# Optimization experiments

Hardware: AMD Instinct MI355X
Metric: run time of the kernel (lower is better)

Reference implementation:

```python
import jax, jax.numpy as jnp
import numpy as np
import math

N_HEAD = 16

def _rope_tables(seq, dh, dtype):
    inv_freq = 1.0 / (10000.0 ** (jnp.arange(0, dh, 2, dtype=jnp.float32) / dh))
    angle = jnp.arange(seq, dtype=jnp.float32)[:, None] * inv_freq[None, :]  # [S, dh/2]
    sin = jnp.repeat(jnp.sin(angle), 2, axis=-1).astype(dtype)  # [S, dh]
    cos = jnp.repeat(jnp.cos(angle), 2, axis=-1).astype(dtype)
    return sin, cos

def _rotate_half(x):
    x_even = x[..., ::2]
    x_odd = x[..., 1::2]
    return jnp.stack([-x_odd, x_even], axis=-1).reshape(x.shape)

def _apply_rope(x, sin, cos):
    # x: [B, H, S, dh]; sin/cos: [S, dh]
    return x * cos[None, None] + _rotate_half(x) * sin[None, None]

def setup_inputs() -> dict:
    key = jax.random.key(0)
    ks = jax.random.split(key, 9)
    B, S, D = 2, 2048, 2048
    scale = 1.0 / math.sqrt(D)
    x = jax.random.normal(ks[0], (B, S, D), dtype=jnp.float32)
    wq = jax.random.normal(ks[1], (D, D), dtype=jnp.float32) * scale
    wk = jax.random.normal(ks[2], (D, D), dtype=jnp.float32) * scale
    wv = jax.random.normal(ks[3], (D, D), dtype=jnp.float32) * scale
    wo = jax.random.normal(ks[4], (D, D), dtype=jnp.float32) * scale
    bq = jnp.zeros((D,), jnp.float32)
    bk = jnp.zeros((D,), jnp.float32)
    bv = jnp.zeros((D,), jnp.float32)
    bo = jnp.zeros((D,), jnp.float32)
    # causal mask: True = masked (strict upper triangle)
    mask = jnp.triu(jnp.ones((S, S), dtype=bool), k=1)[None, None]  # [1,1,S,S]
    return {"x": x, "wq": wq, "bq": bq, "wk": wk, "bk": bk, "wv": wv, "bv": bv,
            "wo": wo, "bo": bo, "mask": mask}

def reference(x, wq, bq, wk, bk, wv, bv, wo, bo, mask):
    B, S, D = x.shape
    H = N_HEAD
    dh = D // H
    # projections (torch Linear: x @ W.T + b)
    q = (x @ wq.T + bq).reshape(B, S, H, dh).transpose(0, 2, 1, 3)  # [B,H,S,dh]
    k = (x @ wk.T + bk).reshape(B, S, H, dh).transpose(0, 2, 1, 3)
    v = (x @ wv.T + bv).reshape(B, S, H, dh).transpose(0, 2, 1, 3)
    sin, cos = _rope_tables(S, dh, x.dtype)
    q = _apply_rope(q, sin, cos)
    k = _apply_rope(k, sin, cos)
    scores = jnp.einsum('bhqd,bhkd->bhqk', q, k) / math.sqrt(dh)
    scores = jnp.where(mask, -jnp.inf, scores)
    attn = jax.nn.softmax(scores, axis=-1)
    attn = jnp.nan_to_num(attn, nan=0.0)
    out = jnp.einsum('bhqk,bhkd->bhqd', attn, v)  # [B,H,S,dh]
    out = out.transpose(0, 2, 1, 3).reshape(B, S, D)
    return out @ wo.T + bo
```

## Files before the change

kernel.cpp:

```cpp
#include <hip/hip_runtime.h>
#include <math.h>


typedef _Float16 half8 __attribute__((ext_vector_type(8)));
typedef _Float16 half4v __attribute__((ext_vector_type(4)));
typedef float f32x4 __attribute__((ext_vector_type(4)));

__device__ __forceinline__ void gl_lds16(const void* g, void* l) {
  __builtin_amdgcn_global_load_lds(
      (const __attribute__((address_space(1))) unsigned int*)g,
      (__attribute__((address_space(3))) unsigned int*)l, 16, 0, 0);
}

__global__ void cast_f32_f16(const float* __restrict__ src, _Float16* __restrict__ dst, int n4) {
  int i = blockIdx.x * blockDim.x + threadIdx.x;
  if (i >= n4) return;
  float4 v = reinterpret_cast<const float4*>(src)[i];
  half4v o;
  o[0] = (_Float16)v.x; o[1] = (_Float16)v.y; o[2] = (_Float16)v.z; o[3] = (_Float16)v.w;
  reinterpret_cast<half4v*>(dst)[i] = o;
}

__global__ void cast_w(const float* __restrict__ w0, const float* __restrict__ w1,
                       const float* __restrict__ w2, const float* __restrict__ w3,
                       _Float16* __restrict__ wdst) {
  const float* s = blockIdx.y == 0 ? w0 : blockIdx.y == 1 ? w1 : blockIdx.y == 2 ? w2 : w3;
  int i = blockIdx.x * blockDim.x + threadIdx.x;
  float4 v = reinterpret_cast<const float4*>(s)[i];
  half4v o;
  o[0] = (_Float16)v.x; o[1] = (_Float16)v.y; o[2] = (_Float16)v.z; o[3] = (_Float16)v.w;
  reinterpret_cast<half4v*>(wdst)[(size_t)blockIdx.y * 1048576 + i] = o;
}

template <bool OUT_F32>
__global__ __launch_bounds__(256, 2) void gemm_bt(
    const _Float16* __restrict__ A,
    const _Float16* __restrict__ B,
    const float* __restrict__ b0, const float* __restrict__ b1,
    const float* __restrict__ b2,
    void* __restrict__ Cout,
    int M, int N, int K) {
  __shared__ _Float16 As[2][4096];
  __shared__ _Float16 Bs[2][4096];
  const int bm = blockIdx.y * 128, bn = blockIdx.x * 128;
  const int tid = threadIdx.x;
  const int wave = tid >> 6, lane = tid & 63;
  const int quad = lane >> 4, l16 = lane & 15;
  const int hh = wave >> 1, gg = wave & 1;

  const _Float16* gsrc[4];
  int lofs[4];
#pragma unroll
  for (int p = 0; p < 4; ++p) {
    int c = ((p & 1) * 256 + tid) & 511;
    int cl16 = c & 15, cqd = (c >> 4) & 3, ci = (c >> 6) & 3, ch = c >> 8;
    int grow = ch * 64 + ci * 16 + cl16;
    int gcol = cqd * 8;
    gsrc[p] = (p < 2 ? A + (size_t)(bm + grow) * K : B + (size_t)(bn + grow) * K) + gcol;
    lofs[p] = c * 8;
  }

  f32x4 acc[4][4];
#pragma unroll
  for (int i = 0; i < 4; ++i)
#pragma unroll
    for (int n = 0; n < 4; ++n) acc[i][n] = f32x4{0.f, 0.f, 0.f, 0.f};

#pragma unroll
  for (int p = 0; p < 4; ++p)
    gl_lds16(gsrc[p], (p < 2 ? &As[0][lofs[p]] : &Bs[0][lofs[p]]));

  const int nit = K >> 5;
  for (int it = 0; it < nit; ++it) {
    __syncthreads();
    const int cur = it & 1;
    if (it + 1 < nit) {
      const int nxt = cur ^ 1, ko = (it + 1) * 32;
#pragma unroll
      for (int p = 0; p < 4; ++p)
        gl_lds16(gsrc[p] + ko, (p < 2 ? &As[nxt][lofs[p]] : &Bs[nxt][lofs[p]]));
    }
    half8 af[4], bf[4];
#pragma unroll
    for (int i = 0; i < 4; ++i)
      af[i] = *reinterpret_cast<const half8*>(&As[cur][((hh * 4 + i) * 4 + quad) * 128 + l16 * 8]);
#pragma unroll
    for (int n = 0; n < 4; ++n)
      bf[n] = *reinterpret_cast<const half8*>(&Bs[cur][((gg * 4 + n) * 4 + quad) * 128 + l16 * 8]);
#pragma unroll
    for (int i = 0; i < 4; ++i)
#pragma unroll
      for (int n = 0; n < 4; ++n)
        acc[i][n] = __builtin_amdgcn_mfma_f32_16x16x32_f16(af[i], bf[n], acc[i][n], 0, 0, 0);
  }

  const int wm = hh * 64, wn = gg * 64;
#pragma unroll
  for (int n = 0; n < 4; ++n) {
    const int gc = bn + wn + n * 16 + l16;
    const float* bp = (gc < 2048) ? b0 : (gc < 4096 ? b1 : b2);
    const float bz = bp[gc & 2047];
#pragma unroll
    for (int i = 0; i < 4; ++i) {
#pragma unroll
      for (int r = 0; r < 4; ++r) {
        const int gr = bm + wm + i * 16 + quad * 4 + r;
        float v = acc[i][n][r] + bz;
        if (OUT_F32)
          reinterpret_cast<float*>(Cout)[(size_t)gr * N + gc] = v;
        else
          reinterpret_cast<_Float16*>(Cout)[(size_t)gr * N + gc] = (_Float16)v;
      }
    }
  }
}

__global__ void rope_inplace(_Float16* __restrict__ qkv, int ngroups) {
  int idx = blockIdx.x * blockDim.x + threadIdx.x;
  if (idx >= ngroups) return;
  int m = idx >> 8;
  int g = idx & 255;
  int s = m & 2047;
  const float scale = 0.088388347648318447f;
  size_t base = (size_t)m * 6144 + g * 8;
  half8 qv = *reinterpret_cast<const half8*>(qkv + base);
  half8 kv = *reinterpret_cast<const half8*>(qkv + base + 2048);
  half8 qo, ko;
#pragma unroll
  for (int j = 0; j < 4; ++j) {
    int i = (g * 4 + j) & 63;
    float ang = (float)s * exp2f(-0.2076205059304601f * (float)i);
    float sn, cs;
    __sincosf(ang, &sn, &cs);
    float e = (float)qv[j * 2], o = (float)qv[j * 2 + 1];
    qo[j * 2]     = (_Float16)((e * cs - o * sn) * scale);
    qo[j * 2 + 1] = (_Float16)((o * cs + e * sn) * scale);
    e = (float)kv[j * 2]; o = (float)kv[j * 2 + 1];
    ko[j * 2]     = (_Float16)(e * cs - o * sn);
    ko[j * 2 + 1] = (_Float16)(o * cs + e * sn);
  }
  *reinterpret_cast<half8*>(qkv + base) = qo;
  *reinterpret_cast<half8*>(qkv + base + 2048) = ko;
}

__global__ __launch_bounds__(256) void transpose_v(const _Float16* __restrict__ qkv,
                                                   _Float16* __restrict__ vt) {
  __shared__ _Float16 t[64][72];
  const int s0 = blockIdx.x * 64;
  const int d0 = blockIdx.y * 64;
  const int bh = blockIdx.z;
  const int b = bh >> 4, h = bh & 15;
  const int tid = threadIdx.x;
#pragma unroll
  for (int p = 0; p < 2; ++p) {
    int chunk = p * 256 + tid;
    int r = chunk >> 3, c8 = (chunk & 7) * 8;
    *reinterpret_cast<half8*>(&t[r][c8]) = *reinterpret_cast<const half8*>(
        &qkv[(size_t)(b * 2048 + s0 + r) * 6144 + 4096 + h * 128 + d0 + c8]);
  }
  __syncthreads();
#pragma unroll
  for (int p = 0; p < 2; ++p) {
    int chunk = p * 256 + tid;
    int dr = chunk >> 3, c8 = (chunk & 7) * 8;
    half8 o;
#pragma unroll
    for (int j = 0; j < 8; ++j) o[j] = t[c8 + j][dr];
    *reinterpret_cast<half8*>(&vt[(size_t)(bh * 128 + d0 + dr) * 2048 + s0 + c8]) = o;
  }
}

__global__ __launch_bounds__(256, 2) void attn_kernel(
    const _Float16* __restrict__ QKV,
    const _Float16* __restrict__ VT,
    _Float16* __restrict__ ctx) {
  constexpr int LD = 6144, S = 2048;
  __shared__ _Float16 Ks[2][8192];
  __shared__ _Float16 Vs[2][8192];
  __shared__ _Float16 P[4][16][80];
  const int bid = blockIdx.x;
  const int bh = bid & 31;
  const int qt = 31 - (bid >> 5);
  const int b = bh >> 4, h = bh & 15;
  const int tid = threadIdx.x;
  const int wv = tid >> 6, lane = tid & 63;
  const int quad = lane >> 4, l16 = lane & 15;
  const int q0 = qt * 64 + wv * 16;

  const _Float16* qp = QKV + (size_t)(b * S + q0 + l16) * LD + h * 128;
  half8 aq[4];
#pragma unroll
  for (int ks = 0; ks < 4; ++ks)
    aq[ks] = *reinterpret_cast<const half8*>(qp + ks * 32 + quad * 8);

  const _Float16* gk[4];
  const _Float16* gv[4];
  int lofs[4];
#pragma unroll
  for (int p = 0; p < 4; ++p) {
    int c = p * 256 + tid;
    int cl16 = c & 15, cqd = (c >> 4) & 3;
    int cks = (c >> 6) & 3, cf = c >> 8;
    gk[p] = QKV + (size_t)(b * S + cf * 16 + cl16) * LD + 2048 + h * 128 + cks * 32 + cqd * 8;
    int ckv = (c >> 6) & 1, ct = c >> 7;
    gv[p] = VT + (size_t)(bh * 128 + ct * 16 + cl16) * S + ckv * 32 + cqd * 8;
    lofs[p] = c * 8;
  }

  f32x4 acc[8];
#pragma unroll
  for (int t = 0; t < 8; ++t) acc[t] = f32x4{0.f, 0.f, 0.f, 0.f};
  f32x4 lacc = f32x4{0.f, 0.f, 0.f, 0.f};
  float m_i[4];
#pragma unroll
  for (int r = 0; r < 4; ++r) m_i[r] = -INFINITY;

  half8 ones;
#pragma unroll
  for (int j = 0; j < 8; ++j) ones[j] = (_Float16)1.0f;

#pragma unroll
  for (int p = 0; p < 4; ++p) gl_lds16(gk[p], &Ks[0][lofs[p]]);
#pragma unroll
  for (int p = 0; p < 4; ++p) gl_lds16(gv[p], &Vs[0][lofs[p]]);

  for (int j = 0; j <= qt; ++j) {
    __syncthreads();
    const int cur = j & 1;
    if (j < qt) {
      const size_t ko = (size_t)(j + 1) * 64 * LD;
      const int vo = (j + 1) * 64;
#pragma unroll
      for (int p = 0; p < 4; ++p) gl_lds16(gk[p] + ko, &Ks[cur ^ 1][lofs[p]]);
#pragma unroll
      for (int p = 0; p < 4; ++p) gl_lds16(gv[p] + vo, &Vs[cur ^ 1][lofs[p]]);
    }
    f32x4 sf[4];
#pragma unroll
    for (int f = 0; f < 4; ++f) sf[f] = f32x4{0.f, 0.f, 0.f, 0.f};
#pragma unroll
    for (int f = 0; f < 4; ++f)
#pragma unroll
      for (int ks = 0; ks < 4; ++ks) {
        half8 bk = *reinterpret_cast<const half8*>(&Ks[cur][((f * 4 + ks) * 4 + quad) * 128 + l16 * 8]);
        sf[f] = __builtin_amdgcn_mfma_f32_16x16x32_f16(aq[ks], bk, sf[f], 0, 0, 0);
      }
    if (j == qt) {
      const int key0 = j * 64;
#pragma unroll
      for (int f = 0; f < 4; ++f) {
        const int key = key0 + f * 16 + l16;
#pragma unroll
        for (int r = 0; r < 4; ++r) {
          const int row = q0 + quad * 4 + r;
          sf[f][r] = (key <= row) ? sf[f][r] : -1e30f;
        }
      }
    }
    float alpha[4];
#pragma unroll
    for (int r = 0; r < 4; ++r) {
      float tm = fmaxf(fmaxf(sf[0][r], sf[1][r]), fmaxf(sf[2][r], sf[3][r]));
      tm = fmaxf(tm, __shfl_xor(tm, 1));
      tm = fmaxf(tm, __shfl_xor(tm, 2));
      tm = fmaxf(tm, __shfl_xor(tm, 4));
      tm = fmaxf(tm, __shfl_xor(tm, 8));
      const float mn = fmaxf(m_i[r], tm);
      alpha[r] = __expf(m_i[r] - mn);
      m_i[r] = mn;
    }
#pragma unroll
    for (int f = 0; f < 4; ++f)
#pragma unroll
      for (int r = 0; r < 4; ++r)
        P[wv][quad * 4 + r][f * 16 + l16] = (_Float16)__expf(sf[f][r] - m_i[r]);
    half8 pa0 = *reinterpret_cast<const half8*>(&P[wv][l16][quad * 8]);
    half8 pa1 = *reinterpret_cast<const half8*>(&P[wv][l16][32 + quad * 8]);
#pragma unroll
    for (int t = 0; t < 8; ++t)
#pragma unroll
      for (int r = 0; r < 4; ++r) acc[t][r] *= alpha[r];
#pragma unroll
    for (int r = 0; r < 4; ++r) lacc[r] *= alpha[r];
#pragma unroll
    for (int t = 0; t < 8; ++t) {
      half8 bv0 = *reinterpret_cast<const half8*>(&Vs[cur][((t * 2 + 0) * 4 + quad) * 128 + l16 * 8]);
      half8 bv1 = *reinterpret_cast<const half8*>(&Vs[cur][((t * 2 + 1) * 4 + quad) * 128 + l16 * 8]);
      acc[t] = __builtin_amdgcn_mfma_f32_16x16x32_f16(pa0, bv0, acc[t], 0, 0, 0);
      acc[t] = __builtin_amdgcn_mfma_f32_16x16x32_f16(pa1, bv1, acc[t], 0, 0, 0);
    }
    lacc = __builtin_amdgcn_mfma_f32_16x16x32_f16(pa0, ones, lacc, 0, 0, 0);
    lacc = __builtin_amdgcn_mfma_f32_16x16x32_f16(pa1, ones, lacc, 0, 0, 0);
  }

  float inv[4];
#pragma unroll
  for (int r = 0; r < 4; ++r) inv[r] = 1.0f / lacc[r];
#pragma unroll
  for (int t = 0; t < 8; ++t)
#pragma unroll
    for (int r = 0; r < 4; ++r)
      ctx[(size_t)(b * S + q0 + quad * 4 + r) * 2048 + h * 128 + t * 16 + l16] =
          (_Float16)(acc[t][r] * inv[r]);
}

extern "C" void kernel_launch(void* const* d_in, const int* in_sizes, int n_in,
                              void* d_out, int out_size, void* d_ws, size_t ws_size,
                              hipStream_t stream) {
  const float* x  = (const float*)d_in[0];
  const float* wq = (const float*)d_in[1];
  const float* bq = (const float*)d_in[2];
  const float* wk = (const float*)d_in[3];
  const float* bk = (const float*)d_in[4];
  const float* wv = (const float*)d_in[5];
  const float* bv = (const float*)d_in[6];
  const float* wo = (const float*)d_in[7];
  const float* bo = (const float*)d_in[8];

  _Float16* W      = (_Float16*)d_ws;
  _Float16* xh     = W;
  _Float16* wqkvh  = xh + 8388608;
  _Float16* woh    = wqkvh + 12582912;
  _Float16* qkvlin = woh + 4194304;
  _Float16* vT     = xh;
  _Float16* ctx    = wqkvh;

  cast_f32_f16<<<8192, 256, 0, stream>>>(x, xh, 2097152);
  cast_w<<<dim3(4096, 4), 256, 0, stream>>>(wq, wk, wv, wo, wqkvh);

  gemm_bt<false><<<dim3(48, 32), 256, 0, stream>>>(xh, wqkvh, bq, bk, bv, qkvlin,
                                                   4096, 6144, 2048);

  rope_inplace<<<4096, 256, 0, stream>>>(qkvlin, 1048576);
  transpose_v<<<dim3(32, 2, 32), 256, 0, stream>>>(qkvlin, vT);
  attn_kernel<<<1024, 256, 0, stream>>>(qkvlin, vT, ctx);

  gemm_bt<true><<<dim3(16, 32), 256, 0, stream>>>(ctx, woh, bo, bo, bo, (float*)d_out,
                                                  4096, 2048, 2048);
}
```

Before: 518.9 us.

## Widen QKV GEMM tile to 128x256 and double attention query rows per block

Adds a gemm_bt_big kernel for the QKV projection that uses a 128x256 output tile, with each wave computing a 64x128 sub-tile (4x8 MFMA fragments). This raises operand reuse from LDS and halves the number of blocks. The attention kernel now gives each wave two 16-row query tiles, so each block covers 128 queries over 512 blocks and every K/V tile loaded into LDS feeds twice as many MFMAs. The trade-off is higher register pressure, fewer blocks (worse causal load balance and tail effects), and waves that skip fully masked key tiles while still taking part in the shared loads.

```diff
diff --git a/kernel.cpp b/kernel.cpp
--- a/kernel.cpp
+++ b/kernel.cpp
@@ -33,7 +33,7 @@
 }
 
 template <bool OUT_F32>
-__global__ __launch_bounds__(256, 2) void gemm_bt(
+__global__ __launch_bounds__(256, 2) void gemm_bt_big(
     const _Float16* __restrict__ A,
     const _Float16* __restrict__ B,
     const float* __restrict__ b0, const float* __restrict__ b1,
@@ -41,6 +41,91 @@
     void* __restrict__ Cout,
     int M, int N, int K) {
   __shared__ _Float16 As[2][4096];
+  __shared__ _Float16 Bs[2][8192];
+  const int bm = blockIdx.y * 128, bn = blockIdx.x * 256;
+  const int tid = threadIdx.x;
+  const int wave = tid >> 6, lane = tid & 63;
+  const int quad = lane >> 4, l16 = lane & 15;
+  const int ih = wave >> 1, jh = wave & 1;
+
+  const _Float16* gsrc[6];
+  int lofs[6];
+#pragma unroll
+  for (int p = 0; p < 6; ++p) {
+    if (p < 2) {
+      int c = p * 256 + tid;
+      int cl16 = c & 15, cqd = (c >> 4) & 3, ci = (c >> 6) & 3, ch = c >> 8;
+      gsrc[p] = A + (size_t)(bm + ch * 64 + ci * 16 + cl16) * K + cqd * 8;
+      lofs[p] = c * 8;
+    } else {
+      int c = (p - 2) * 256 + tid;
+      int cl16 = c & 15, cqd = (c >> 4) & 3, cn = (c >> 6) & 7, cjh = (c >> 9) & 1;
+      gsrc[p] = B + (size_t)(bn + cjh * 128 + cn * 16 + cl16) * K + cqd * 8;
+      lofs[p] = c * 8;
+    }
+  }
+
+  f32x4 acc[4][8];
+#pragma unroll
+  for (int i = 0; i < 4; ++i)
+#pragma unroll
+    for (int n = 0; n < 8; ++n) acc[i][n] = f32x4{0.f, 0.f, 0.f, 0.f};
+
+#pragma unroll
+  for (int p = 0; p < 6; ++p)
+    gl_lds16(gsrc[p], (p < 2 ? &As[0][lofs[p]] : &Bs[0][lofs[p]]));
+
+  const int nit = K >> 5;
+  for (int it = 0; it < nit; ++it) {
+    __syncthreads();
+    const int cur = it & 1;
+    if (it + 1 < nit) {
+      const int nxt = cur ^ 1, ko = (it + 1) * 32;
+#pragma unroll
+      for (int p = 0; p < 6; ++p)
+        gl_lds16(gsrc[p] + ko, (p < 2 ? &As[nxt][lofs[p]] : &Bs[nxt][lofs[p]]));
+    }
+    half8 af[4], bf[8];
+#pragma unroll
+    for (int i = 0; i < 4; ++i)
+      af[i] = *reinterpret_cast<const half8*>(&As[cur][((ih * 4 + i) * 4 + quad) * 128 + l16 * 8]);
+#pragma unroll
+    for (int n = 0; n < 8; ++n)
+      bf[n] = *reinterpret_cast<const half8*>(&Bs[cur][((jh * 8 + n) * 4 + quad) * 128 + l16 * 8]);
+#pragma unroll
+    for (int i = 0; i < 4; ++i)
+#pragma unroll
+      for (int n = 0; n < 8; ++n)
+        acc[i][n] = __builtin_amdgcn_mfma_f32_16x16x32_f16(af[i], bf[n], acc[i][n], 0, 0, 0);
+  }
+
+  const int wm = ih * 64, wn = jh * 128;
+#pragma unroll
+  for (int n = 0; n < 8; ++n) {
+    const int gc = bn + wn + n * 16 + l16;
+    const float* bp = (gc < 2048) ? b0 : (gc < 4096 ? b1 : b2);
+    const float bz = bp[gc & 2047];
+#pragma unroll
+    for (int i = 0; i < 4; ++i) {
+#pragma unroll
+      for (int r = 0; r < 4; ++r) {
+        const int gr = bm + wm + i * 16 + quad * 4 + r;
+        float v = acc[i][n][r] + bz;
+        if (OUT_F32)
+          reinterpret_cast<float*>(Cout)[(size_t)gr * N + gc] = v;
+        else
+          reinterpret_cast<_Float16*>(Cout)[(size_t)gr * N + gc] = (_Float16)v;
+      }
+    }
+  }
+}
+
+template <bool OUT_F32>
+__global__ __launch_bounds__(256, 2) void gemm_bt(
+    const _Float16* __restrict__ A, const _Float16* __restrict__ B,
+    const float* __restrict__ b0, const float* __restrict__ b1,
+    const float* __restrict__ b2, void* __restrict__ Cout, int M, int N, int K) {
+  __shared__ _Float16 As[2][4096];
   __shared__ _Float16 Bs[2][4096];
   const int bm = blockIdx.y * 128, bn = blockIdx.x * 128;
   const int tid = threadIdx.x;
@@ -55,8 +140,7 @@
     int c = ((p & 1) * 256 + tid) & 511;
     int cl16 = c & 15, cqd = (c >> 4) & 3, ci = (c >> 6) & 3, ch = c >> 8;
     int grow = ch * 64 + ci * 16 + cl16;
-    int gcol = cqd * 8;
-    gsrc[p] = (p < 2 ? A + (size_t)(bm + grow) * K : B + (size_t)(bn + grow) * K) + gcol;
+    gsrc[p] = (p < 2 ? A + (size_t)(bm + grow) * K : B + (size_t)(bn + grow) * K) + cqd * 8;
     lofs[p] = c * 8;
   }
 
@@ -180,18 +264,20 @@
   __shared__ _Float16 P[4][16][80];
   const int bid = blockIdx.x;
   const int bh = bid & 31;
-  const int qt = 31 - (bid >> 5);
+  const int qt = 15 - (bid >> 5);
   const int b = bh >> 4, h = bh & 15;
   const int tid = threadIdx.x;
   const int wv = tid >> 6, lane = tid & 63;
   const int quad = lane >> 4, l16 = lane & 15;
-  const int q0 = qt * 64 + wv * 16;
-
-  const _Float16* qp = QKV + (size_t)(b * S + q0 + l16) * LD + h * 128;
-  half8 aq[4];
-#pragma unroll
-  for (int ks = 0; ks < 4; ++ks)
-    aq[ks] = *reinterpret_cast<const half8*>(qp + ks * 32 + quad * 8);
+  const int q0 = qt * 128 + wv * 32;
+
+  half8 aq[2][4];
+#pragma unroll
+  for (int rt = 0; rt < 2; ++rt)
+#pragma unroll
+    for (int ks = 0; ks < 4; ++ks)
+      aq[rt][ks] = *reinterpret_cast<const half8*>(
+          QKV + (size_t)(b * S + q0 + rt * 16 + l16) * LD + h * 128 + ks * 32 + quad * 8);
 
   const _Float16* gk[4];
   const _Float16* gv[4];
@@ -207,13 +293,17 @@
     lofs[p] = c * 8;
   }
 
-  f32x4 acc[8];
-#pragma unroll
-  for (int t = 0; t < 8; ++t) acc[t] = f32x4{0.f, 0.f, 0.f, 0.f};
-  f32x4 lacc = f32x4{0.f, 0.f, 0.f, 0.f};
-  float m_i[4];
-#pragma unroll
-  for (int r = 0; r < 4; ++r) m_i[r] = -INFINITY;
+  f32x4 acc[2][8];
+#pragma unroll
+  for (int rt = 0; rt < 2; ++rt)
+#pragma unroll
+    for (int t = 0; t < 8; ++t) acc[rt][t] = f32x4{0.f, 0.f, 0.f, 0.f};
+  f32x4 lacc[2] = {f32x4{0.f, 0.f, 0.f, 0.f}, f32x4{0.f, 0.f, 0.f, 0.f}};
+  float m_i[2][4];
+#pragma unroll
+  for (int rt = 0; rt < 2; ++rt)
+#pragma unroll
+    for (int r = 0; r < 4; ++r) m_i[rt][r] = -INFINITY;
 
   half8 ones;
 #pragma unroll
@@ -224,10 +314,11 @@
 #pragma unroll
   for (int p = 0; p < 4; ++p) gl_lds16(gv[p], &Vs[0][lofs[p]]);
 
-  for (int j = 0; j <= qt; ++j) {
+  const int nkt = 2 * (qt + 1);
+  for (int j = 0; j < nkt; ++j) {
     __syncthreads();
     const int cur = j & 1;
-    if (j < qt) {
+    if (j + 1 < nkt) {
       const size_t ko = (size_t)(j + 1) * 64 * LD;
       const int vo = (j + 1) * 64;
 #pragma unroll
@@ -235,73 +326,96 @@
 #pragma unroll
       for (int p = 0; p < 4; ++p) gl_lds16(gv[p] + vo, &Vs[cur ^ 1][lofs[p]]);
     }
-    f32x4 sf[4];
-#pragma unroll
-    for (int f = 0; f < 4; ++f) sf[f] = f32x4{0.f, 0.f, 0.f, 0.f};
+    const int key0 = j * 64;
+    if (key0 > q0 + 31) continue;
+
+    f32x4 sf[2][4];
+#pragma unroll
+    for (int rt = 0; rt < 2; ++rt)
+#pragma unroll
+      for (int f = 0; f < 4; ++f) sf[rt][f] = f32x4{0.f, 0.f, 0.f, 0.f};
 #pragma unroll
     for (int f = 0; f < 4; ++f)
 #pragma unroll
       for (int ks = 0; ks < 4; ++ks) {
         half8 bk = *reinterpret_cast<const half8*>(&Ks[cur][((f * 4 + ks) * 4 + quad) * 128 + l16 * 8]);
-        sf[f] = __builtin_amdgcn_mfma_f32_16x16x32_f16(aq[ks], bk, sf[f], 0, 0, 0);
+        sf[0][f] = __builtin_amdgcn_mfma_f32_16x16x32_f16(aq[0][ks], bk, sf[0][f], 0, 0, 0);
+        sf[1][f] = __builtin_amdgcn_mfma_f32_16x16x32_f16(aq[1][ks], bk, sf[1][f], 0, 0, 0);
       }
-    if (j == qt) {
-      const int key0 = j * 64;
-#pragma unroll
-      for (int f = 0; f < 4; ++f) {
-        const int key = key0 + f * 16 + l16;
-#pragma unroll
-        for (int r = 0; r < 4; ++r) {
-          const int row = q0 + quad * 4 + r;
-          sf[f][r] = (key <= row) ? sf[f][r] : -1e30f;
+    if (key0 + 63 > q0) {
+#pragma unroll
+      for (int rt = 0; rt < 2; ++rt)
+#pragma unroll
+        for (int f = 0; f < 4; ++f) {
+          const int key = key0 + f * 16 + l16;
+#pragma unroll
+          for (int r = 0; r < 4; ++r) {
+            const int row = q0 + rt * 16 + quad * 4 + r;
+            sf[rt][f][r] = (key <= row) ? sf[rt][f][r] : -1e30f;
+          }
         }
+    }
+    float alpha[2][4];
+    half8 pa[2][2];
+#pragma unroll
+    for (int rt = 0; rt < 2; ++rt) {
+#pragma unroll
+      for (int r = 0; r < 4; ++r) {
+        float tm = fmaxf(fmaxf(sf[rt][0][r], sf[rt][1][r]), fmaxf(sf[rt][2][r], sf[rt][3][r]));
+        tm = fmaxf(tm, __shfl_xor(tm, 1));
+        tm = fmaxf(tm, __shfl_xor(tm, 2));
+        tm = fmaxf(tm, __shfl_xor(tm, 4));
+        tm = fmaxf(tm, __shfl_xor(tm, 8));
+        const float mn = fmaxf(m_i[rt][r], tm);
+        alpha[rt][r] = __expf(m_i[rt][r] - mn);
+        m_i[rt][r] = mn;
       }
-    }
-    float alpha[4];
-#pragma unroll
-    for (int r = 0; r < 4; ++r) {
-      float tm = fmaxf(fmaxf(sf[0][r], sf[1][r]), fmaxf(sf[2][r], sf[3][r]));
-      tm = fmaxf(tm, __shfl_xor(tm, 1));
-      tm = fmaxf(tm, __shfl_xor(tm, 2));
-      tm = fmaxf(tm, __shfl_xor(tm, 4));
-      tm = fmaxf(tm, __shfl_xor(tm, 8));
-      const float mn = fmaxf(m_i[r], tm);
-      alpha[r] = __expf(m_i[r] - mn);
-      m_i[r] = mn;
-    }
-#pragma unroll
-    for (int f = 0; f < 4; ++f)
-#pragma unroll
-      for (int r = 0; r < 4; ++r)
-        P[wv][quad * 4 + r][f * 16 + l16] = (_Float16)__expf(sf[f][r] - m_i[r]);
-    half8 pa0 = *reinterpret_cast<const half8*>(&P[wv][l16][quad * 8]);
-    half8 pa1 = *reinterpret_cast<const half8*>(&P[wv][l16][32 + quad * 8]);
-#pragma unroll
-    for (int t = 0; t < 8; ++t)
-#pragma unroll
-      for (int r = 0; r < 4; ++r) acc[t][r] *= alpha[r];
-#pragma unroll
-    for (int r = 0; r < 4; ++r) lacc[r] *= alpha[r];
+#pragma unroll
+      for (int f = 0; f < 4; ++f)
+#pragma unroll
+        for (int r = 0; r < 4; ++r)
+          P[wv][quad * 4 + r][f * 16 + l16] = (_Float16)__expf(sf[rt][f][r] - m_i[rt][r]);
+      pa[rt][0] = *reinterpret_cast<const half8*>(&P[wv][l16][quad * 8]);
+      pa[rt][1] = *reinterpret_cast<const half8*>(&P[wv][l16][32 + quad * 8]);
+    }
+#pragma unroll
+    for (int rt = 0; rt < 2; ++rt) {
+#pragma unroll
+      for (int t = 0; t < 8; ++t)
+#pragma unroll
+        for (int r = 0; r < 4; ++r) acc[rt][t][r] *= alpha[rt][r];
+#pragma unroll
+      for (int r = 0; r < 4; ++r) lacc[rt][r] *= alpha[rt][r];
+    }
 #pragma unroll
     for (int t = 0; t < 8; ++t) {
       half8 bv0 = *reinterpret_cast<const half8*>(&Vs[cur][((t * 2 + 0) * 4 + quad) * 128 + l16 * 8]);
       half8 bv1 = *reinterpret_cast<const half8*>(&Vs[cur][((t * 2 + 1) * 4 + quad) * 128 + l16 * 8]);
-      acc[t] = __builtin_amdgcn_mfma_f32_16x16x32_f16(pa0, bv0, acc[t], 0, 0, 0);
-      acc[t] = __builtin_amdgcn_mfma_f32_16x16x32_f16(pa1, bv1, acc[t], 0, 0, 0);
-    }
-    lacc = __builtin_amdgcn_mfma_f32_16x16x32_f16(pa0, ones, lacc, 0, 0, 0);
-    lacc = __builtin_amdgcn_mfma_f32_16x16x32_f16(pa1, ones, lacc, 0, 0, 0);
-  }
-
-  float inv[4];
-#pragma unroll
-  for (int r = 0; r < 4; ++r) inv[r] = 1.0f / lacc[r];
-#pragma unroll
-  for (int t = 0; t < 8; ++t)
-#pragma unroll
-    for (int r = 0; r < 4; ++r)
-      ctx[(size_t)(b * S + q0 + quad * 4 + r) * 2048 + h * 128 + t * 16 + l16] =
-          (_Float16)(acc[t][r] * inv[r]);
+#pragma unroll
+      for (int rt = 0; rt < 2; ++rt) {
+        acc[rt][t] = __builtin_amdgcn_mfma_f32_16x16x32_f16(pa[rt][0], bv0, acc[rt][t], 0, 0, 0);
+        acc[rt][t] = __builtin_amdgcn_mfma_f32_16x16x32_f16(pa[rt][1], bv1, acc[rt][t], 0, 0, 0);
+      }
+    }
+#pragma unroll
+    for (int rt = 0; rt < 2; ++rt) {
+      lacc[rt] = __builtin_amdgcn_mfma_f32_16x16x32_f16(pa[rt][0], ones, lacc[rt], 0, 0, 0);
+      lacc[rt] = __builtin_amdgcn_mfma_f32_16x16x32_f16(pa[rt][1], ones, lacc[rt], 0, 0, 0);
+    }
+  }
+
+#pragma unroll
+  for (int rt = 0; rt < 2; ++rt) {
+    float inv[4];
+#pragma unroll
+    for (int r = 0; r < 4; ++r) inv[r] = 1.0f / lacc[rt][r];
+#pragma unroll
+    for (int t = 0; t < 8; ++t)
+#pragma unroll
+      for (int r = 0; r < 4; ++r)
+        ctx[(size_t)(b * S + q0 + rt * 16 + quad * 4 + r) * 2048 + h * 128 + t * 16 + l16] =
+            (_Float16)(acc[rt][t][r] * inv[r]);
+  }
 }
 
 extern "C" void kernel_launch(void* const* d_in, const int* in_sizes, int n_in,
@@ -328,12 +442,12 @@
   cast_f32_f16<<<8192, 256, 0, stream>>>(x, xh, 2097152);
   cast_w<<<dim3(4096, 4), 256, 0, stream>>>(wq, wk, wv, wo, wqkvh);
 
-  gemm_bt<false><<<dim3(48, 32), 256, 0, stream>>>(xh, wqkvh, bq, bk, bv, qkvlin,
-                                                   4096, 6144, 2048);
+  gemm_bt_big<false><<<dim3(24, 32), 256, 0, stream>>>(xh, wqkvh, bq, bk, bv, qkvlin,
+                                                       4096, 6144, 2048);
 
   rope_inplace<<<4096, 256, 0, stream>>>(qkvlin, 1048576);
   transpose_v<<<dim3(32, 2, 32), 256, 0, stream>>>(qkvlin, vT);
-  attn_kernel<<<1024, 256, 0, stream>>>(qkvlin, vT, ctx);
+  attn_kernel<<<512, 256, 0, stream>>>(qkvlin, vT, ctx);
 
   gemm_bt<true><<<dim3(16, 32), 256, 0, stream>>>(ctx, woh, bo, bo, bo, (float*)d_out,
                                                   4096, 2048, 2048);
```

Result: no change. 526.1 us (+1.4%).
